# Optimization experiments

Hardware: AMD Instinct MI355X
Metric: run time of the kernel (lower is better)

The kernel has to match this reference:

```python
import jax, jax.numpy as jnp
import numpy as np

EPS = 1e-5  # torch BatchNorm2d default eps


def _bn(x, gamma, beta, mean, var):
    # x: (B, C, H, W); params: (C,). Inference-mode batch norm (running stats).
    inv = gamma / jnp.sqrt(var + EPS)
    return x * inv[:, None, None] + (beta - mean * inv)[:, None, None]


def setup_inputs() -> dict:
    key = jax.random.key(0)
    ks = jax.random.split(key, 8)
    B, QC, QH, QW = 8, 64, 64, 64
    VC, VH, VW = 128, 32, 32
    q = jax.random.normal(ks[0], (B, QC, QH, QW), dtype=jnp.float32)
    v = jax.random.normal(ks[1], (B, VC, VH, VW), dtype=jnp.float32)
    # 1x1 conv weights (out_ch, in_ch), bias=False
    k_w = jax.random.normal(ks[2], (QC, VC), dtype=jnp.float32) * (1.0 / np.sqrt(VC))
    v_w = jax.random.normal(ks[3], (QC, VC), dtype=jnp.float32) * (1.0 / np.sqrt(VC))
    # BatchNorm params (inference mode with running stats)
    q_gamma = jnp.ones((QC,), jnp.float32)
    q_beta = jnp.zeros((QC,), jnp.float32)
    q_mean = jax.random.normal(ks[4], (QC,), dtype=jnp.float32) * 0.1
    q_var = jax.random.uniform(ks[5], (QC,), dtype=jnp.float32, minval=0.5, maxval=1.5)
    k_gamma = jnp.ones((QC,), jnp.float32)
    k_beta = jnp.zeros((QC,), jnp.float32)
    k_mean = jax.random.normal(ks[6], (QC,), dtype=jnp.float32) * 0.1
    k_var = jax.random.uniform(ks[7], (QC,), dtype=jnp.float32, minval=0.5, maxval=1.5)
    return {
        "q": q, "v": v, "k_w": k_w, "v_w": v_w,
        "q_gamma": q_gamma, "q_beta": q_beta, "q_mean": q_mean, "q_var": q_var,
        "k_gamma": k_gamma, "k_beta": k_beta, "k_mean": k_mean, "k_var": k_var,
    }


def reference(q, v, k_w, v_w, q_gamma, q_beta, q_mean, q_var,
              k_gamma, k_beta, k_mean, k_var):
    B, C, H, W = q.shape
    Nq = H * W
    # query: BN(q) -> (B, Nq, C)
    qn = _bn(q, q_gamma, q_beta, q_mean, q_var)
    query = qn.reshape(B, C, Nq).transpose(0, 2, 1)
    # key: 1x1 conv + BN -> (B, C, Nv)
    key = jnp.einsum('oc,bchw->bohw', k_w, v)
    key = _bn(key, k_gamma, k_beta, k_mean, k_var)
    Nv = key.shape[2] * key.shape[3]
    key = key.reshape(B, C, Nv)
    # value: 1x1 conv -> (B, Nv, C)
    value = jnp.einsum('oc,bchw->bohw', v_w, v).reshape(B, C, Nv).transpose(0, 2, 1)
    # full spatial attention (NO 1/sqrt(d) scaling, matching source)
    sim = jnp.einsum('bnc,bcm->bnm', query, key)          # (B, Nq, Nv)
    attn = jax.nn.softmax(sim, axis=-1)
    out = jnp.einsum('bnm,bmc->bnc', attn, value)         # (B, Nq, C)
    return out.transpose(0, 2, 1).reshape(B, C, H, W)
```

## Files before the change

### kernel.cpp

```cpp
#include <hip/hip_runtime.h>
#include <hip/hip_bf16.h>

#define EPS 1e-5f

typedef _Float16 f16x8 __attribute__((ext_vector_type(8)));
typedef short short8v __attribute__((ext_vector_type(8)));
typedef float f32x4 __attribute__((ext_vector_type(4)));

static __device__ __forceinline__ unsigned short f2h(float x) {
    _Float16 h = (_Float16)x;
    return *reinterpret_cast<unsigned short*>(&h);
}

__global__ __launch_bounds__(256) void conv_kv_kernel(const float* __restrict__ v,
                               const float* __restrict__ k_w, const float* __restrict__ v_w,
                               const float* __restrict__ kg, const float* __restrict__ kbe,
                               const float* __restrict__ km, const float* __restrict__ kvv,
                               unsigned short* __restrict__ Kt, unsigned short* __restrict__ Vt) {
    __shared__ unsigned short vtile[32 * 136];
    const int t = threadIdx.x;
    const int w = t >> 6, lane = t & 63, g = lane >> 4, qr = lane & 15;
    const int b = blockIdx.y, m0 = blockIdx.x * 32;

    float4 vstg[4];
#pragma unroll
    for (int r = 0; r < 4; ++r) {
        int idx = r * 256 + t;
        int c = idx >> 3, mq = idx & 7;
        vstg[r] = *reinterpret_cast<const float4*>(&v[((size_t)b * 128 + c) * 1024 + m0 + mq * 4]);
    }
    float4 kwl[4][2], vwl[4][2];
#pragma unroll
    for (int ck = 0; ck < 4; ++ck) {
        const float* kp = &k_w[(16 * w + qr) * 128 + 32 * ck + 8 * g];
        const float* vp = &v_w[(16 * w + qr) * 128 + 32 * ck + 8 * g];
        kwl[ck][0] = *reinterpret_cast<const float4*>(kp);
        kwl[ck][1] = *reinterpret_cast<const float4*>(kp + 4);
        vwl[ck][0] = *reinterpret_cast<const float4*>(vp);
        vwl[ck][1] = *reinterpret_cast<const float4*>(vp + 4);
    }
#pragma unroll
    for (int r = 0; r < 4; ++r) {
        int idx = r * 256 + t;
        int c = idx >> 3, mq = idx & 7;
        vtile[(mq * 4 + 0) * 136 + c] = f2h(vstg[r].x);
        vtile[(mq * 4 + 1) * 136 + c] = f2h(vstg[r].y);
        vtile[(mq * 4 + 2) * 136 + c] = f2h(vstg[r].z);
        vtile[(mq * 4 + 3) * 136 + c] = f2h(vstg[r].w);
    }
    __syncthreads();

    f16x8 kwf[4], vwf[4];
#pragma unroll
    for (int ck = 0; ck < 4; ++ck)
#pragma unroll
        for (int j = 0; j < 8; ++j) {
            kwf[ck][j] = (_Float16)(j < 4 ? kwl[ck][0][j] : kwl[ck][1][j - 4]);
            vwf[ck][j] = (_Float16)(j < 4 ? vwl[ck][0][j] : vwl[ck][1][j - 4]);
        }

    f32x4 accK[2], accV[2];
#pragma unroll
    for (int mb = 0; mb < 2; ++mb) {
        f16x8 bf[4];
#pragma unroll
        for (int ck = 0; ck < 4; ++ck)
            bf[ck] = *reinterpret_cast<const f16x8*>(&vtile[(mb * 16 + qr) * 136 + 32 * ck + 8 * g]);
        f32x4 aK = {0.f, 0.f, 0.f, 0.f}, aV = {0.f, 0.f, 0.f, 0.f};
#pragma unroll
        for (int ck = 0; ck < 4; ++ck) {
            aK = __builtin_amdgcn_mfma_f32_16x16x32_f16(kwf[ck], bf[ck], aK, 0, 0, 0);
            aV = __builtin_amdgcn_mfma_f32_16x16x32_f16(vwf[ck], bf[ck], aV, 0, 0, 0);
        }
        accK[mb] = aK; accV[mb] = aV;
    }

    float invk_i[4], biask_i[4];
#pragma unroll
    for (int i = 0; i < 4; ++i) {
        int o = 16 * w + 4 * g + i;
        invk_i[i] = kg[o] * rsqrtf(kvv[o] + EPS);
        biask_i[i] = kbe[o] - km[o] * invk_i[i];
    }
#pragma unroll
    for (int mb = 0; mb < 2; ++mb) {
        int m = m0 + mb * 16 + qr;
#pragma unroll
        for (int i = 0; i < 4; ++i) {
            int o = 16 * w + 4 * g + i;
            Kt[((size_t)b * 1024 + m) * 64 + o] = f2h(accK[mb][i] * invk_i[i] + biask_i[i]);
            Vt[((size_t)b * 64 + o) * 1024 + m] = f2h(accV[mb][i]);
        }
    }
}

__global__ __launch_bounds__(256, 2) void attn_kernel(const float* __restrict__ q,
        const float* __restrict__ qg, const float* __restrict__ qbt,
        const float* __restrict__ qm, const float* __restrict__ qv,
        const unsigned short* __restrict__ Kt, const unsigned short* __restrict__ Vt,
        float* __restrict__ out) {
    __shared__ __align__(16) unsigned char smem[45568];
    unsigned short* S16 = (unsigned short*)smem;
    float* SF = (float*)smem;
    const int t = threadIdx.x;
    const int w = t >> 6, lane = t & 63, g = lane >> 4, qr = lane & 15;
    const int p = w & 1, h = w >> 1;
    const int b = blockIdx.y, n0 = blockIdx.x * 64;

    unsigned short* kT = S16 + w * 4864;
    unsigned short* vT = kT + 2304;
    unsigned short* pT = S16 + 19456 + w * 640;
    float* ib  = SF + 11008;
    float* mlb = SF + 11136;

    const int koff0 = h * 512;
    const int kr_row = lane >> 3, kr_sub = lane & 7;
    const int vr_row = lane >> 2, vr_sub = lane & 3;

    short8v kpf[4], vpf[4];
#pragma unroll
    for (int ch = 0; ch < 4; ++ch) {
        kpf[ch] = *reinterpret_cast<const short8v*>(
            Kt + (size_t)(b * 1024 + koff0 + ch * 8 + kr_row) * 64 + kr_sub * 8);
        vpf[ch] = *reinterpret_cast<const short8v*>(
            Vt + (size_t)(b * 64 + ch * 16 + vr_row) * 1024 + koff0 + vr_sub * 8);
    }

    if (t < 64) {
        float inv = qg[t] * rsqrtf(qv[t] + EPS);
        ib[t] = inv * 1.44269504f;
        ib[64 + t] = (qbt[t] - qm[t] * inv) * 1.44269504f;
    }
    __syncthreads();

    const int nqA = n0 + p * 32 + qr, nqB = nqA + 16;
    f16x8 qfA0, qfA1, qfB0, qfB1;
#pragma unroll
    for (int j = 0; j < 8; ++j) {
        int c0 = g * 8 + j, c1 = 32 + g * 8 + j;
        qfA0[j] = (_Float16)(q[(size_t)(b * 64 + c0) * 4096 + nqA] * ib[c0] + ib[64 + c0]);
        qfA1[j] = (_Float16)(q[(size_t)(b * 64 + c1) * 4096 + nqA] * ib[c1] + ib[64 + c1]);
        qfB0[j] = (_Float16)(q[(size_t)(b * 64 + c0) * 4096 + nqB] * ib[c0] + ib[64 + c0]);
        qfB1[j] = (_Float16)(q[(size_t)(b * 64 + c1) * 4096 + nqB] * ib[c1] + ib[64 + c1]);
    }

#pragma unroll
    for (int ch = 0; ch < 4; ++ch) {
        *reinterpret_cast<short8v*>(kT + (ch * 8 + kr_row) * 72 + kr_sub * 8) = kpf[ch];
        *reinterpret_cast<short8v*>(vT + (ch * 16 + vr_row) * 40 + vr_sub * 8) = vpf[ch];
    }

    f32x4 oaccA[4], oaccB[4];
#pragma unroll
    for (int cb = 0; cb < 4; ++cb) { oaccA[cb] = (f32x4){0,0,0,0}; oaccB[cb] = (f32x4){0,0,0,0}; }
    float mrA = -1e30f, mrB = -1e30f, lpA = 0.f, lpB = 0.f;

    auto body = [&](const f16x8& q0, const f16x8& q1, f32x4 (&oa)[4], float& mr, float& lp) {
        f32x4 s0, s1;
        {
            f16x8 kf0 = *reinterpret_cast<const f16x8*>(kT + qr * 72 + g * 8);
            f16x8 kf1 = *reinterpret_cast<const f16x8*>(kT + qr * 72 + 32 + g * 8);
            f32x4 a = {0,0,0,0};
            a  = __builtin_amdgcn_mfma_f32_16x16x32_f16(kf0, q0, a, 0, 0, 0);
            s0 = __builtin_amdgcn_mfma_f32_16x16x32_f16(kf1, q1, a, 0, 0, 0);
        }
        {
            f16x8 kf0 = *reinterpret_cast<const f16x8*>(kT + (16 + qr) * 72 + g * 8);
            f16x8 kf1 = *reinterpret_cast<const f16x8*>(kT + (16 + qr) * 72 + 32 + g * 8);
            f32x4 a = {0,0,0,0};
            a  = __builtin_amdgcn_mfma_f32_16x16x32_f16(kf0, q0, a, 0, 0, 0);
            s1 = __builtin_amdgcn_mfma_f32_16x16x32_f16(kf1, q1, a, 0, 0, 0);
        }
        float lmax = fmaxf(fmaxf(fmaxf(s0[0], s0[1]), fmaxf(s0[2], s0[3])),
                           fmaxf(fmaxf(s1[0], s1[1]), fmaxf(s1[2], s1[3])));
        if (!__all(lmax - mr <= 11.0f)) {
            float tm = fmaxf(lmax, __shfl_xor(lmax, 16));
            tm = fmaxf(tm, __shfl_xor(tm, 32));
            float mn = fmaxf(mr, tm);
            float sc = exp2f(mr - mn);
            lp *= sc;
            oa[0] *= sc; oa[1] *= sc; oa[2] *= sc; oa[3] *= sc;
            mr = mn;
        }
        float p0 = exp2f(s0[0] - mr), p1 = exp2f(s0[1] - mr);
        float p2 = exp2f(s0[2] - mr), p3 = exp2f(s0[3] - mr);
        float p4 = exp2f(s1[0] - mr), p5 = exp2f(s1[1] - mr);
        float p6 = exp2f(s1[2] - mr), p7 = exp2f(s1[3] - mr);
        lp += ((p0 + p1) + (p2 + p3)) + ((p4 + p5) + (p6 + p7));
        uint2 w0, w1;
        w0.x = __builtin_bit_cast(unsigned int, __builtin_amdgcn_cvt_pkrtz(p0, p1));
        w0.y = __builtin_bit_cast(unsigned int, __builtin_amdgcn_cvt_pkrtz(p2, p3));
        w1.x = __builtin_bit_cast(unsigned int, __builtin_amdgcn_cvt_pkrtz(p4, p5));
        w1.y = __builtin_bit_cast(unsigned int, __builtin_amdgcn_cvt_pkrtz(p6, p7));
        *reinterpret_cast<uint2*>(pT + qr * 40 + g * 4) = w0;
        *reinterpret_cast<uint2*>(pT + qr * 40 + 16 + g * 4) = w1;
        f16x8 pf = *reinterpret_cast<const f16x8*>(pT + qr * 40 + g * 8);
#pragma unroll
        for (int cb = 0; cb < 4; ++cb) {
            f16x8 vf = *reinterpret_cast<const f16x8*>(vT + (cb * 16 + qr) * 40 + g * 8);
            oa[cb] = __builtin_amdgcn_mfma_f32_16x16x32_f16(vf, pf, oa[cb], 0, 0, 0);
        }
    };

#pragma unroll 1
    for (int i = 0; i < 16; ++i) {
        if (i < 15) {
            int ko = koff0 + (i + 1) * 32;
#pragma unroll
            for (int ch = 0; ch < 4; ++ch) {
                kpf[ch] = *reinterpret_cast<const short8v*>(
                    Kt + (size_t)(b * 1024 + ko + ch * 8 + kr_row) * 64 + kr_sub * 8);
                vpf[ch] = *reinterpret_cast<const short8v*>(
                    Vt + (size_t)(b * 64 + ch * 16 + vr_row) * 1024 + ko + vr_sub * 8);
            }
        }
        body(qfA0, qfA1, oaccA, mrA, lpA);
        body(qfB0, qfB1, oaccB, mrB, lpB);
        if (i < 15) {
#pragma unroll
            for (int ch = 0; ch < 4; ++ch) {
                *reinterpret_cast<short8v*>(kT + (ch * 8 + kr_row) * 72 + kr_sub * 8) = kpf[ch];
                *reinterpret_cast<short8v*>(vT + (ch * 16 + vr_row) * 40 + vr_sub * 8) = vpf[ch];
            }
        }
    }

    float lA = lpA + __shfl_xor(lpA, 16); lA += __shfl_xor(lA, 32);
    float lB = lpB + __shfl_xor(lpB, 16); lB += __shfl_xor(lB, 32);
    __syncthreads();
    float* ob = SF + w * 2176;
#pragma unroll
    for (int cb = 0; cb < 4; ++cb) {
        *reinterpret_cast<f32x4*>(&ob[qr * 68 + cb * 16 + g * 4]) = oaccA[cb];
        *reinterpret_cast<f32x4*>(&ob[(16 + qr) * 68 + cb * 16 + g * 4]) = oaccB[cb];
    }
    if (g == 0) {
        mlb[w * 64 + qr * 2] = mrA;        mlb[w * 64 + qr * 2 + 1] = lA;
        mlb[w * 64 + (16 + qr) * 2] = mrB; mlb[w * 64 + (16 + qr) * 2 + 1] = lB;
    }
    __syncthreads();
    const int p2 = w & 1, hh = w >> 1;
    const int rowrel = hh * 16 + qr;
    const float* o0 = SF + p2 * 2176 + rowrel * 68;
    const float* o1 = SF + (2 + p2) * 2176 + rowrel * 68;
    float m0 = mlb[p2 * 64 + rowrel * 2],       l0 = mlb[p2 * 64 + rowrel * 2 + 1];
    float m1 = mlb[(2 + p2) * 64 + rowrel * 2], l1 = mlb[(2 + p2) * 64 + rowrel * 2 + 1];
    float M = fmaxf(m0, m1);
    float w0 = exp2f(m0 - M), w1 = exp2f(m1 - M);
    float rd = 1.0f / (w0 * l0 + w1 * l1);
    const int nout = n0 + p2 * 32 + rowrel;
#pragma unroll
    for (int j = 0; j < 16; ++j) {
        int c = j * 4 + g;
        out[(size_t)(b * 64 + c) * 4096 + nout] = (o0[c] * w0 + o1[c] * w1) * rd;
    }
}

extern "C" void kernel_launch(void* const* d_in, const int* in_sizes, int n_in,
                              void* d_out, int out_size, void* d_ws, size_t ws_size,
                              hipStream_t stream) {
    const float* q   = (const float*)d_in[0];
    const float* v   = (const float*)d_in[1];
    const float* k_w = (const float*)d_in[2];
    const float* v_w = (const float*)d_in[3];
    const float* qg  = (const float*)d_in[4];
    const float* qb  = (const float*)d_in[5];
    const float* qm  = (const float*)d_in[6];
    const float* qv  = (const float*)d_in[7];
    const float* kg  = (const float*)d_in[8];
    const float* kbe = (const float*)d_in[9];
    const float* km  = (const float*)d_in[10];
    const float* kvv = (const float*)d_in[11];

    unsigned short* Kt = (unsigned short*)d_ws;
    unsigned short* Vt = Kt + (size_t)8 * 1024 * 64;

    conv_kv_kernel<<<dim3(32, 8), 256, 0, stream>>>(v, k_w, v_w, kg, kbe, km, kvv, Kt, Vt);
    attn_kernel<<<dim3(64, 8), 256, 0, stream>>>(q, qg, qb, qm, qv, Kt, Vt, (float*)d_out);
}
```

Before: 39.17 us.

## Halve queries per block, pass P via shuffles instead of LDS, raise occupancy

Each wave now handles 16 query rows instead of 32, so the grid doubles to 1024 blocks and launch bounds are raised to 4 blocks per CU. The P tile goes from MFMA output layout to operand layout through lane shuffles rather than an LDS round-trip, which frees the pT buffer and shrinks shared memory. The aim is more parallelism and latency hiding on a small problem and less LDS traffic. The cost is that each block loads K/V tiles for half as many queries, doubling K/V global traffic, plus extra shuffle instructions.

```diff
diff --git a/kernel.cpp b/kernel.cpp
--- a/kernel.cpp
+++ b/kernel.cpp
@@ -6,6 +6,7 @@
 typedef _Float16 f16x8 __attribute__((ext_vector_type(8)));
 typedef short short8v __attribute__((ext_vector_type(8)));
 typedef float f32x4 __attribute__((ext_vector_type(4)));
+typedef unsigned int uint4v __attribute__((ext_vector_type(4)));
 
 static __device__ __forceinline__ unsigned short f2h(float x) {
     _Float16 h = (_Float16)x;
@@ -94,24 +95,23 @@
     }
 }
 
-__global__ __launch_bounds__(256, 2) void attn_kernel(const float* __restrict__ q,
+__global__ __launch_bounds__(256, 4) void attn_kernel(const float* __restrict__ q,
         const float* __restrict__ qg, const float* __restrict__ qbt,
         const float* __restrict__ qm, const float* __restrict__ qv,
         const unsigned short* __restrict__ Kt, const unsigned short* __restrict__ Vt,
         float* __restrict__ out) {
-    __shared__ __align__(16) unsigned char smem[45568];
+    __shared__ __align__(16) unsigned char smem[39936];
     unsigned short* S16 = (unsigned short*)smem;
     float* SF = (float*)smem;
     const int t = threadIdx.x;
     const int w = t >> 6, lane = t & 63, g = lane >> 4, qr = lane & 15;
     const int p = w & 1, h = w >> 1;
-    const int b = blockIdx.y, n0 = blockIdx.x * 64;
+    const int b = blockIdx.y, n0 = blockIdx.x * 32;
 
     unsigned short* kT = S16 + w * 4864;
     unsigned short* vT = kT + 2304;
-    unsigned short* pT = S16 + 19456 + w * 640;
-    float* ib  = SF + 11008;
-    float* mlb = SF + 11136;
+    float* ib  = SF + 9728;
+    float* mlb = SF + 9856;
 
     const int koff0 = h * 512;
     const int kr_row = lane >> 3, kr_sub = lane & 7;
@@ -133,15 +133,13 @@
     }
     __syncthreads();
 
-    const int nqA = n0 + p * 32 + qr, nqB = nqA + 16;
-    f16x8 qfA0, qfA1, qfB0, qfB1;
+    const int nq = n0 + p * 16 + qr;
+    f16x8 qf0, qf1;
 #pragma unroll
     for (int j = 0; j < 8; ++j) {
         int c0 = g * 8 + j, c1 = 32 + g * 8 + j;
-        qfA0[j] = (_Float16)(q[(size_t)(b * 64 + c0) * 4096 + nqA] * ib[c0] + ib[64 + c0]);
-        qfA1[j] = (_Float16)(q[(size_t)(b * 64 + c1) * 4096 + nqA] * ib[c1] + ib[64 + c1]);
-        qfB0[j] = (_Float16)(q[(size_t)(b * 64 + c0) * 4096 + nqB] * ib[c0] + ib[64 + c0]);
-        qfB1[j] = (_Float16)(q[(size_t)(b * 64 + c1) * 4096 + nqB] * ib[c1] + ib[64 + c1]);
+        qf0[j] = (_Float16)(q[(size_t)(b * 64 + c0) * 4096 + nq] * ib[c0] + ib[64 + c0]);
+        qf1[j] = (_Float16)(q[(size_t)(b * 64 + c1) * 4096 + nq] * ib[c1] + ib[64 + c1]);
     }
 
 #pragma unroll
@@ -150,26 +148,38 @@
         *reinterpret_cast<short8v*>(vT + (ch * 16 + vr_row) * 40 + vr_sub * 8) = vpf[ch];
     }
 
-    f32x4 oaccA[4], oaccB[4];
-#pragma unroll
-    for (int cb = 0; cb < 4; ++cb) { oaccA[cb] = (f32x4){0,0,0,0}; oaccB[cb] = (f32x4){0,0,0,0}; }
-    float mrA = -1e30f, mrB = -1e30f, lpA = 0.f, lpB = 0.f;
-
-    auto body = [&](const f16x8& q0, const f16x8& q1, f32x4 (&oa)[4], float& mr, float& lp) {
+    f32x4 oacc[4];
+#pragma unroll
+    for (int cb = 0; cb < 4; ++cb) oacc[cb] = (f32x4){0, 0, 0, 0};
+    float mr = -1e30f, lp = 0.f;
+    const int srcA = qr + ((g & 1) << 5), srcB = srcA + 16;
+
+#pragma unroll 1
+    for (int i = 0; i < 16; ++i) {
+        if (i < 15) {
+            int ko = koff0 + (i + 1) * 32;
+#pragma unroll
+            for (int ch = 0; ch < 4; ++ch) {
+                kpf[ch] = *reinterpret_cast<const short8v*>(
+                    Kt + (size_t)(b * 1024 + ko + ch * 8 + kr_row) * 64 + kr_sub * 8);
+                vpf[ch] = *reinterpret_cast<const short8v*>(
+                    Vt + (size_t)(b * 64 + ch * 16 + vr_row) * 1024 + ko + vr_sub * 8);
+            }
+        }
         f32x4 s0, s1;
         {
             f16x8 kf0 = *reinterpret_cast<const f16x8*>(kT + qr * 72 + g * 8);
             f16x8 kf1 = *reinterpret_cast<const f16x8*>(kT + qr * 72 + 32 + g * 8);
-            f32x4 a = {0,0,0,0};
-            a  = __builtin_amdgcn_mfma_f32_16x16x32_f16(kf0, q0, a, 0, 0, 0);
-            s0 = __builtin_amdgcn_mfma_f32_16x16x32_f16(kf1, q1, a, 0, 0, 0);
+            f32x4 a = {0, 0, 0, 0};
+            a  = __builtin_amdgcn_mfma_f32_16x16x32_f16(kf0, qf0, a, 0, 0, 0);
+            s0 = __builtin_amdgcn_mfma_f32_16x16x32_f16(kf1, qf1, a, 0, 0, 0);
         }
         {
             f16x8 kf0 = *reinterpret_cast<const f16x8*>(kT + (16 + qr) * 72 + g * 8);
             f16x8 kf1 = *reinterpret_cast<const f16x8*>(kT + (16 + qr) * 72 + 32 + g * 8);
-            f32x4 a = {0,0,0,0};
-            a  = __builtin_amdgcn_mfma_f32_16x16x32_f16(kf0, q0, a, 0, 0, 0);
-            s1 = __builtin_amdgcn_mfma_f32_16x16x32_f16(kf1, q1, a, 0, 0, 0);
+            f32x4 a = {0, 0, 0, 0};
+            a  = __builtin_amdgcn_mfma_f32_16x16x32_f16(kf0, qf0, a, 0, 0, 0);
+            s1 = __builtin_amdgcn_mfma_f32_16x16x32_f16(kf1, qf1, a, 0, 0, 0);
         }
         float lmax = fmaxf(fmaxf(fmaxf(s0[0], s0[1]), fmaxf(s0[2], s0[3])),
                            fmaxf(fmaxf(s1[0], s1[1]), fmaxf(s1[2], s1[3])));
@@ -179,7 +189,7 @@
             float mn = fmaxf(mr, tm);
             float sc = exp2f(mr - mn);
             lp *= sc;
-            oa[0] *= sc; oa[1] *= sc; oa[2] *= sc; oa[3] *= sc;
+            oacc[0] *= sc; oacc[1] *= sc; oacc[2] *= sc; oacc[3] *= sc;
             mr = mn;
         }
         float p0 = exp2f(s0[0] - mr), p1 = exp2f(s0[1] - mr);
@@ -187,35 +197,24 @@
         float p4 = exp2f(s1[0] - mr), p5 = exp2f(s1[1] - mr);
         float p6 = exp2f(s1[2] - mr), p7 = exp2f(s1[3] - mr);
         lp += ((p0 + p1) + (p2 + p3)) + ((p4 + p5) + (p6 + p7));
-        uint2 w0, w1;
-        w0.x = __builtin_bit_cast(unsigned int, __builtin_amdgcn_cvt_pkrtz(p0, p1));
-        w0.y = __builtin_bit_cast(unsigned int, __builtin_amdgcn_cvt_pkrtz(p2, p3));
-        w1.x = __builtin_bit_cast(unsigned int, __builtin_amdgcn_cvt_pkrtz(p4, p5));
-        w1.y = __builtin_bit_cast(unsigned int, __builtin_amdgcn_cvt_pkrtz(p6, p7));
-        *reinterpret_cast<uint2*>(pT + qr * 40 + g * 4) = w0;
-        *reinterpret_cast<uint2*>(pT + qr * 40 + 16 + g * 4) = w1;
-        f16x8 pf = *reinterpret_cast<const f16x8*>(pT + qr * 40 + g * 8);
+        int w0x = __builtin_bit_cast(int, __builtin_amdgcn_cvt_pkrtz(p0, p1));
+        int w0y = __builtin_bit_cast(int, __builtin_amdgcn_cvt_pkrtz(p2, p3));
+        int w1x = __builtin_bit_cast(int, __builtin_amdgcn_cvt_pkrtz(p4, p5));
+        int w1y = __builtin_bit_cast(int, __builtin_amdgcn_cvt_pkrtz(p6, p7));
+        int a0 = __shfl(w0x, srcA), a1 = __shfl(w0y, srcA);
+        int a2 = __shfl(w0x, srcB), a3 = __shfl(w0y, srcB);
+        int b0 = __shfl(w1x, srcA), b1 = __shfl(w1y, srcA);
+        int b2 = __shfl(w1x, srcB), b3 = __shfl(w1y, srcB);
+        bool lo = (g < 2);
+        uint4v pw;
+        pw[0] = lo ? a0 : b0; pw[1] = lo ? a1 : b1;
+        pw[2] = lo ? a2 : b2; pw[3] = lo ? a3 : b3;
+        f16x8 pf = __builtin_bit_cast(f16x8, pw);
 #pragma unroll
         for (int cb = 0; cb < 4; ++cb) {
             f16x8 vf = *reinterpret_cast<const f16x8*>(vT + (cb * 16 + qr) * 40 + g * 8);
-            oa[cb] = __builtin_amdgcn_mfma_f32_16x16x32_f16(vf, pf, oa[cb], 0, 0, 0);
-        }
-    };
-
-#pragma unroll 1
-    for (int i = 0; i < 16; ++i) {
-        if (i < 15) {
-            int ko = koff0 + (i + 1) * 32;
-#pragma unroll
-            for (int ch = 0; ch < 4; ++ch) {
-                kpf[ch] = *reinterpret_cast<const short8v*>(
-                    Kt + (size_t)(b * 1024 + ko + ch * 8 + kr_row) * 64 + kr_sub * 8);
-                vpf[ch] = *reinterpret_cast<const short8v*>(
-                    Vt + (size_t)(b * 64 + ch * 16 + vr_row) * 1024 + ko + vr_sub * 8);
-            }
-        }
-        body(qfA0, qfA1, oaccA, mrA, lpA);
-        body(qfB0, qfB1, oaccB, mrB, lpB);
+            oacc[cb] = __builtin_amdgcn_mfma_f32_16x16x32_f16(vf, pf, oacc[cb], 0, 0, 0);
+        }
         if (i < 15) {
 #pragma unroll
             for (int ch = 0; ch < 4; ++ch) {
@@ -225,34 +224,31 @@
         }
     }
 
-    float lA = lpA + __shfl_xor(lpA, 16); lA += __shfl_xor(lA, 32);
-    float lB = lpB + __shfl_xor(lpB, 16); lB += __shfl_xor(lB, 32);
-    __syncthreads();
-    float* ob = SF + w * 2176;
-#pragma unroll
-    for (int cb = 0; cb < 4; ++cb) {
-        *reinterpret_cast<f32x4*>(&ob[qr * 68 + cb * 16 + g * 4]) = oaccA[cb];
-        *reinterpret_cast<f32x4*>(&ob[(16 + qr) * 68 + cb * 16 + g * 4]) = oaccB[cb];
-    }
+    float l = lp + __shfl_xor(lp, 16); l += __shfl_xor(l, 32);
+    __syncthreads();
+    float* ob = SF + w * 1088;
+#pragma unroll
+    for (int cb = 0; cb < 4; ++cb)
+        *reinterpret_cast<f32x4*>(&ob[qr * 68 + cb * 16 + g * 4]) = oacc[cb];
     if (g == 0) {
-        mlb[w * 64 + qr * 2] = mrA;        mlb[w * 64 + qr * 2 + 1] = lA;
-        mlb[w * 64 + (16 + qr) * 2] = mrB; mlb[w * 64 + (16 + qr) * 2 + 1] = lB;
+        mlb[w * 32 + qr * 2] = mr;
+        mlb[w * 32 + qr * 2 + 1] = l;
     }
     __syncthreads();
     const int p2 = w & 1, hh = w >> 1;
-    const int rowrel = hh * 16 + qr;
-    const float* o0 = SF + p2 * 2176 + rowrel * 68;
-    const float* o1 = SF + (2 + p2) * 2176 + rowrel * 68;
-    float m0 = mlb[p2 * 64 + rowrel * 2],       l0 = mlb[p2 * 64 + rowrel * 2 + 1];
-    float m1 = mlb[(2 + p2) * 64 + rowrel * 2], l1 = mlb[(2 + p2) * 64 + rowrel * 2 + 1];
+    const int row = lane & 15;
+    const float* o0 = SF + p2 * 1088 + row * 68;
+    const float* o1 = SF + (2 + p2) * 1088 + row * 68;
+    float m0 = mlb[p2 * 32 + row * 2],       l0 = mlb[p2 * 32 + row * 2 + 1];
+    float m1 = mlb[(2 + p2) * 32 + row * 2], l1 = mlb[(2 + p2) * 32 + row * 2 + 1];
     float M = fmaxf(m0, m1);
-    float w0 = exp2f(m0 - M), w1 = exp2f(m1 - M);
-    float rd = 1.0f / (w0 * l0 + w1 * l1);
-    const int nout = n0 + p2 * 32 + rowrel;
-#pragma unroll
-    for (int j = 0; j < 16; ++j) {
-        int c = j * 4 + g;
-        out[(size_t)(b * 64 + c) * 4096 + nout] = (o0[c] * w0 + o1[c] * w1) * rd;
+    float w0e = exp2f(m0 - M), w1e = exp2f(m1 - M);
+    float rd = 1.0f / (w0e * l0 + w1e * l1);
+    const int nout = n0 + p2 * 16 + row;
+#pragma unroll
+    for (int j = 0; j < 8; ++j) {
+        int c = hh * 32 + g * 8 + j;
+        out[(size_t)(b * 64 + c) * 4096 + nout] = (o0[c] * w0e + o1[c] * w1e) * rd;
     }
 }
 
@@ -276,5 +272,5 @@
     unsigned short* Vt = Kt + (size_t)8 * 1024 * 64;
 
     conv_kv_kernel<<<dim3(32, 8), 256, 0, stream>>>(v, k_w, v_w, kg, kbe, km, kvv, Kt, Vt);
-    attn_kernel<<<dim3(64, 8), 256, 0, stream>>>(q, qg, qb, qm, qv, Kt, Vt, (float*)d_out);
-}
+    attn_kernel<<<dim3(128, 8), 256, 0, stream>>>(q, qg, qb, qm, qv, Kt, Vt, (float*)d_out);
+}
```

After: 44.69 us. +14.1%, slower.

## Split KV across all four waves, each wave handling all 64 query rows

Applied to the files above, without the earlier changes.

Each wave now processes all 64 queries of the block against a quarter of the keys, instead of a 2x2 split of queries and key halves. Each K/V tile loaded into shared memory is reused across four query subtiles, which cuts global K/V traffic per query. The cost is a four-way softmax merge, done as a serialized accumulation into shared memory with extra barriers, plus more registers (16 accumulators) and more LDS. The larger LDS footprint and register pressure may limit the two-blocks-per-CU occupancy target.

```diff
diff --git a/kernel.cpp b/kernel.cpp
--- a/kernel.cpp
+++ b/kernel.cpp
@@ -99,21 +99,19 @@
         const float* __restrict__ qm, const float* __restrict__ qv,
         const unsigned short* __restrict__ Kt, const unsigned short* __restrict__ Vt,
         float* __restrict__ out) {
-    __shared__ __align__(16) unsigned char smem[45568];
+    __shared__ __align__(16) unsigned char smem[61952];
     unsigned short* S16 = (unsigned short*)smem;
     float* SF = (float*)smem;
     const int t = threadIdx.x;
     const int w = t >> 6, lane = t & 63, g = lane >> 4, qr = lane & 15;
-    const int p = w & 1, h = w >> 1;
     const int b = blockIdx.y, n0 = blockIdx.x * 64;
 
     unsigned short* kT = S16 + w * 4864;
     unsigned short* vT = kT + 2304;
-    unsigned short* pT = S16 + 19456 + w * 640;
-    float* ib  = SF + 11008;
-    float* mlb = SF + 11136;
-
-    const int koff0 = h * 512;
+    float* ib  = SF + 14848;
+    float* mlb = SF + 14976;
+
+    const int koff0 = w * 256;
     const int kr_row = lane >> 3, kr_sub = lane & 7;
     const int vr_row = lane >> 2, vr_sub = lane & 3;
 
@@ -133,15 +131,16 @@
     }
     __syncthreads();
 
-    const int nqA = n0 + p * 32 + qr, nqB = nqA + 16;
-    f16x8 qfA0, qfA1, qfB0, qfB1;
-#pragma unroll
-    for (int j = 0; j < 8; ++j) {
-        int c0 = g * 8 + j, c1 = 32 + g * 8 + j;
-        qfA0[j] = (_Float16)(q[(size_t)(b * 64 + c0) * 4096 + nqA] * ib[c0] + ib[64 + c0]);
-        qfA1[j] = (_Float16)(q[(size_t)(b * 64 + c1) * 4096 + nqA] * ib[c1] + ib[64 + c1]);
-        qfB0[j] = (_Float16)(q[(size_t)(b * 64 + c0) * 4096 + nqB] * ib[c0] + ib[64 + c0]);
-        qfB1[j] = (_Float16)(q[(size_t)(b * 64 + c1) * 4096 + nqB] * ib[c1] + ib[64 + c1]);
+    f16x8 qf0[4], qf1[4];
+#pragma unroll
+    for (int j = 0; j < 4; ++j) {
+        int nq = n0 + j * 16 + qr;
+#pragma unroll
+        for (int e = 0; e < 8; ++e) {
+            int c0 = g * 8 + e, c1 = 32 + g * 8 + e;
+            qf0[j][e] = (_Float16)(q[(size_t)(b * 64 + c0) * 4096 + nq] * ib[c0] + ib[64 + c0]);
+            qf1[j][e] = (_Float16)(q[(size_t)(b * 64 + c1) * 4096 + nq] * ib[c1] + ib[64 + c1]);
+        }
     }
 
 #pragma unroll
@@ -150,61 +149,66 @@
         *reinterpret_cast<short8v*>(vT + (ch * 16 + vr_row) * 40 + vr_sub * 8) = vpf[ch];
     }
 
-    f32x4 oaccA[4], oaccB[4];
-#pragma unroll
-    for (int cb = 0; cb < 4; ++cb) { oaccA[cb] = (f32x4){0,0,0,0}; oaccB[cb] = (f32x4){0,0,0,0}; }
-    float mrA = -1e30f, mrB = -1e30f, lpA = 0.f, lpB = 0.f;
-
-    auto body = [&](const f16x8& q0, const f16x8& q1, f32x4 (&oa)[4], float& mr, float& lp) {
+    f32x4 oacc[4][4];
+#pragma unroll
+    for (int j = 0; j < 4; ++j)
+#pragma unroll
+        for (int cb = 0; cb < 4; ++cb) oacc[j][cb] = (f32x4){0, 0, 0, 0};
+    float mr[4] = {-1e30f, -1e30f, -1e30f, -1e30f};
+    float lp[4] = {0.f, 0.f, 0.f, 0.f};
+
+    auto body = [&](int j, unsigned short* pTj) {
         f32x4 s0, s1;
         {
             f16x8 kf0 = *reinterpret_cast<const f16x8*>(kT + qr * 72 + g * 8);
             f16x8 kf1 = *reinterpret_cast<const f16x8*>(kT + qr * 72 + 32 + g * 8);
-            f32x4 a = {0,0,0,0};
-            a  = __builtin_amdgcn_mfma_f32_16x16x32_f16(kf0, q0, a, 0, 0, 0);
-            s0 = __builtin_amdgcn_mfma_f32_16x16x32_f16(kf1, q1, a, 0, 0, 0);
+            f32x4 a = {0, 0, 0, 0};
+            a  = __builtin_amdgcn_mfma_f32_16x16x32_f16(kf0, qf0[j], a, 0, 0, 0);
+            s0 = __builtin_amdgcn_mfma_f32_16x16x32_f16(kf1, qf1[j], a, 0, 0, 0);
         }
         {
             f16x8 kf0 = *reinterpret_cast<const f16x8*>(kT + (16 + qr) * 72 + g * 8);
             f16x8 kf1 = *reinterpret_cast<const f16x8*>(kT + (16 + qr) * 72 + 32 + g * 8);
-            f32x4 a = {0,0,0,0};
-            a  = __builtin_amdgcn_mfma_f32_16x16x32_f16(kf0, q0, a, 0, 0, 0);
-            s1 = __builtin_amdgcn_mfma_f32_16x16x32_f16(kf1, q1, a, 0, 0, 0);
+            f32x4 a = {0, 0, 0, 0};
+            a  = __builtin_amdgcn_mfma_f32_16x16x32_f16(kf0, qf0[j], a, 0, 0, 0);
+            s1 = __builtin_amdgcn_mfma_f32_16x16x32_f16(kf1, qf1[j], a, 0, 0, 0);
         }
         float lmax = fmaxf(fmaxf(fmaxf(s0[0], s0[1]), fmaxf(s0[2], s0[3])),
                            fmaxf(fmaxf(s1[0], s1[1]), fmaxf(s1[2], s1[3])));
-        if (!__all(lmax - mr <= 11.0f)) {
+        if (!__all(lmax - mr[j] <= 11.0f)) {
             float tm = fmaxf(lmax, __shfl_xor(lmax, 16));
             tm = fmaxf(tm, __shfl_xor(tm, 32));
-            float mn = fmaxf(mr, tm);
-            float sc = exp2f(mr - mn);
-            lp *= sc;
-            oa[0] *= sc; oa[1] *= sc; oa[2] *= sc; oa[3] *= sc;
-            mr = mn;
-        }
-        float p0 = exp2f(s0[0] - mr), p1 = exp2f(s0[1] - mr);
-        float p2 = exp2f(s0[2] - mr), p3 = exp2f(s0[3] - mr);
-        float p4 = exp2f(s1[0] - mr), p5 = exp2f(s1[1] - mr);
-        float p6 = exp2f(s1[2] - mr), p7 = exp2f(s1[3] - mr);
-        lp += ((p0 + p1) + (p2 + p3)) + ((p4 + p5) + (p6 + p7));
+            float mn = fmaxf(mr[j], tm);
+            float sc = exp2f(mr[j] - mn);
+            lp[j] *= sc;
+            oacc[j][0] *= sc; oacc[j][1] *= sc; oacc[j][2] *= sc; oacc[j][3] *= sc;
+            mr[j] = mn;
+        }
+        float p0 = exp2f(s0[0] - mr[j]), p1 = exp2f(s0[1] - mr[j]);
+        float p2 = exp2f(s0[2] - mr[j]), p3 = exp2f(s0[3] - mr[j]);
+        float p4 = exp2f(s1[0] - mr[j]), p5 = exp2f(s1[1] - mr[j]);
+        float p6 = exp2f(s1[2] - mr[j]), p7 = exp2f(s1[3] - mr[j]);
+        lp[j] += ((p0 + p1) + (p2 + p3)) + ((p4 + p5) + (p6 + p7));
         uint2 w0, w1;
         w0.x = __builtin_bit_cast(unsigned int, __builtin_amdgcn_cvt_pkrtz(p0, p1));
         w0.y = __builtin_bit_cast(unsigned int, __builtin_amdgcn_cvt_pkrtz(p2, p3));
         w1.x = __builtin_bit_cast(unsigned int, __builtin_amdgcn_cvt_pkrtz(p4, p5));
         w1.y = __builtin_bit_cast(unsigned int, __builtin_amdgcn_cvt_pkrtz(p6, p7));
-        *reinterpret_cast<uint2*>(pT + qr * 40 + g * 4) = w0;
-        *reinterpret_cast<uint2*>(pT + qr * 40 + 16 + g * 4) = w1;
-        f16x8 pf = *reinterpret_cast<const f16x8*>(pT + qr * 40 + g * 8);
+        *reinterpret_cast<uint2*>(pTj + qr * 40 + g * 4) = w0;
+        *reinterpret_cast<uint2*>(pTj + qr * 40 + 16 + g * 4) = w1;
+        f16x8 pf = *reinterpret_cast<const f16x8*>(pTj + qr * 40 + g * 8);
 #pragma unroll
         for (int cb = 0; cb < 4; ++cb) {
             f16x8 vf = *reinterpret_cast<const f16x8*>(vT + (cb * 16 + qr) * 40 + g * 8);
-            oa[cb] = __builtin_amdgcn_mfma_f32_16x16x32_f16(vf, pf, oa[cb], 0, 0, 0);
+            oacc[j][cb] = __builtin_amdgcn_mfma_f32_16x16x32_f16(vf, pf, oacc[j][cb], 0, 0, 0);
         }
     };
 
+    unsigned short* pTbase = S16 + 19456 + w * 2560;
+
 #pragma unroll 1
-    for (int i = 0; i < 16; ++i) {
-        if (i < 15) {
+    for (int i = 0; i < 8; ++i) {
+        if (i < 7) {
             int ko = koff0 + (i + 1) * 32;
 #pragma unroll
             for (int ch = 0; ch < 4; ++ch) {
@@ -214,9 +218,11 @@
                     Vt + (size_t)(b * 64 + ch * 16 + vr_row) * 1024 + ko + vr_sub * 8);
             }
         }
-        body(qfA0, qfA1, oaccA, mrA, lpA);
-        body(qfB0, qfB1, oaccB, mrB, lpB);
-        if (i < 15) {
+        body(0, pTbase);
+        body(1, pTbase + 640);
+        body(2, pTbase + 1280);
+        body(3, pTbase + 1920);
+        if (i < 7) {
 #pragma unroll
             for (int ch = 0; ch < 4; ++ch) {
                 *reinterpret_cast<short8v*>(kT + (ch * 8 + kr_row) * 72 + kr_sub * 8) = kpf[ch];
@@ -225,34 +231,63 @@
         }
     }
 
-    float lA = lpA + __shfl_xor(lpA, 16); lA += __shfl_xor(lA, 32);
-    float lB = lpB + __shfl_xor(lpB, 16); lB += __shfl_xor(lB, 32);
+    float lred[4];
+#pragma unroll
+    for (int j = 0; j < 4; ++j) {
+        float l = lp[j] + __shfl_xor(lp[j], 16);
+        lred[j] = l + __shfl_xor(l, 32);
+    }
     __syncthreads();
-    float* ob = SF + w * 2176;
-#pragma unroll
-    for (int cb = 0; cb < 4; ++cb) {
-        *reinterpret_cast<f32x4*>(&ob[qr * 68 + cb * 16 + g * 4]) = oaccA[cb];
-        *reinterpret_cast<f32x4*>(&ob[(16 + qr) * 68 + cb * 16 + g * 4]) = oaccB[cb];
-    }
     if (g == 0) {
-        mlb[w * 64 + qr * 2] = mrA;        mlb[w * 64 + qr * 2 + 1] = lA;
-        mlb[w * 64 + (16 + qr) * 2] = mrB; mlb[w * 64 + (16 + qr) * 2 + 1] = lB;
+#pragma unroll
+        for (int j = 0; j < 4; ++j) {
+            mlb[((w * 4 + j) * 16 + qr) * 2] = mr[j];
+            mlb[((w * 4 + j) * 16 + qr) * 2 + 1] = lred[j];
+        }
     }
     __syncthreads();
-    const int p2 = w & 1, hh = w >> 1;
-    const int rowrel = hh * 16 + qr;
-    const float* o0 = SF + p2 * 2176 + rowrel * 68;
-    const float* o1 = SF + (2 + p2) * 2176 + rowrel * 68;
-    float m0 = mlb[p2 * 64 + rowrel * 2],       l0 = mlb[p2 * 64 + rowrel * 2 + 1];
-    float m1 = mlb[(2 + p2) * 64 + rowrel * 2], l1 = mlb[(2 + p2) * 64 + rowrel * 2 + 1];
-    float M = fmaxf(m0, m1);
-    float w0 = exp2f(m0 - M), w1 = exp2f(m1 - M);
-    float rd = 1.0f / (w0 * l0 + w1 * l1);
-    const int nout = n0 + p2 * 32 + rowrel;
-#pragma unroll
-    for (int j = 0; j < 16; ++j) {
-        int c = j * 4 + g;
-        out[(size_t)(b * 64 + c) * 4096 + nout] = (o0[c] * w0 + o1[c] * w1) * rd;
+    float scale_j[4];
+#pragma unroll
+    for (int j = 0; j < 4; ++j) {
+        float m0 = mlb[((0 * 4 + j) * 16 + qr) * 2], l0 = mlb[((0 * 4 + j) * 16 + qr) * 2 + 1];
+        float m1 = mlb[((1 * 4 + j) * 16 + qr) * 2], l1 = mlb[((1 * 4 + j) * 16 + qr) * 2 + 1];
+        float m2 = mlb[((2 * 4 + j) * 16 + qr) * 2], l2 = mlb[((2 * 4 + j) * 16 + qr) * 2 + 1];
+        float m3 = mlb[((3 * 4 + j) * 16 + qr) * 2], l3 = mlb[((3 * 4 + j) * 16 + qr) * 2 + 1];
+        float M = fmaxf(fmaxf(m0, m1), fmaxf(m2, m3));
+        float e0 = exp2f(m0 - M), e1 = exp2f(m1 - M), e2 = exp2f(m2 - M), e3 = exp2f(m3 - M);
+        float L = e0 * l0 + e1 * l1 + e2 * l2 + e3 * l3;
+        float ew = (w == 0) ? e0 : (w == 1) ? e1 : (w == 2) ? e2 : e3;
+        scale_j[j] = ew / L;
+#pragma unroll
+        for (int cb = 0; cb < 4; ++cb) oacc[j][cb] *= scale_j[j];
+    }
+    float* ob = SF;
+#pragma unroll 1
+    for (int r = 0; r < 4; ++r) {
+        if (w == r) {
+#pragma unroll
+            for (int j = 0; j < 4; ++j)
+#pragma unroll
+                for (int cb = 0; cb < 4; ++cb) {
+                    float* dst = &ob[(j * 16 + qr) * 68 + cb * 16 + g * 4];
+                    if (r == 0) *reinterpret_cast<f32x4*>(dst) = oacc[j][cb];
+                    else {
+                        f32x4 cur = *reinterpret_cast<const f32x4*>(dst);
+                        *reinterpret_cast<f32x4*>(dst) = cur + oacc[j][cb];
+                    }
+                }
+        }
+        __syncthreads();
+    }
+    const int row = lane;
+#pragma unroll
+    for (int k = 0; k < 4; ++k) {
+        f32x4 val = *reinterpret_cast<const f32x4*>(&ob[row * 68 + w * 16 + k * 4]);
+#pragma unroll
+        for (int e = 0; e < 4; ++e) {
+            int c = w * 16 + k * 4 + e;
+            out[(size_t)(b * 64 + c) * 4096 + n0 + row] = val[e];
+        }
     }
 }
 
```

Measured after the change: 40.27 us. 2.8% more time.
